# Performance work log

Measured on AMD Instinct MI355X. Metric: run time of the kernel, lower is better.

Reference implementation:

```python
import jax, jax.numpy as jnp
import numpy as np

L = 43          # number of classes
C = L + 3       # <eps>, 'O', 'I-', + L class symbols
B = 128
T = 4096
NEG = jnp.float32(-1e30)


def setup_inputs() -> dict:
    key = jax.random.key(0)
    k1, k2, k3, k4 = jax.random.split(key, 4)
    logits = jax.random.normal(k1, (B, T, C), dtype=jnp.float32)
    log_probs = jax.nn.log_softmax(logits, axis=-1)
    input_lens = jax.random.randint(k2, (B,), T // 2, T + 1).astype(jnp.int32)
    labels = jax.random.randint(k3, (B, T), 1, C).astype(jnp.int32)  # valid (non-eps) symbols
    # den_scores parameter: one raw score per denominator arc (2L+4 arcs).
    # Layout: [0]=0->0 'O', [1:L+1]=0->0 labels, [L+1]=0->1 'I-', [L+2]=0->final,
    #         [L+3]=1->1 'I-', [L+4:2L+4]=1->0 labels.
    den_params = 0.01 * jax.random.normal(k4, (2 * L + 4,), dtype=jnp.float32)
    return {"log_probs": log_probs, "den_params": den_params,
            "input_lens": input_lens, "labels": labels}


def reference(log_probs, den_params, input_lens, labels):
    Bb, Tt, Cc = log_probs.shape
    Ll = Cc - 3
    # set_scores_stochastic_: per-source-state log-softmax of arc scores
    g0 = jax.nn.log_softmax(den_params[: Ll + 3])   # state-0 outgoing arcs
    g1 = jax.nn.log_softmax(den_params[Ll + 3:])    # state-1 outgoing arcs
    s_O, s0_lab, s_0I, s_fin = g0[0], g0[1:Ll + 1], g0[Ll + 1], g0[Ll + 2]
    s_1I, s1_lab = g1[0], g1[1:]

    mask = jnp.arange(Tt)[None, :] < input_lens[:, None]          # [B,T]

    # ---- numerator: linear FSA intersected with emissions = path score ----
    tok_lp = jnp.take_along_axis(log_probs, labels[..., None], axis=-1)[..., 0]
    num = jnp.sum(jnp.where(mask, tok_lp, 0.0), axis=1)           # [B]

    # ---- denominator: log-semiring forward DP over the 2-state topology ----
    lp_t = jnp.moveaxis(log_probs, 1, 0)    # [T,B,C]
    mask_t = jnp.moveaxis(mask, 1, 0)       # [T,B]

    def step(alpha, inputs):
        lp, m = inputs                       # lp [B,C], m [B]
        a0, a1 = alpha[:, 0], alpha[:, 1]
        lp_lab = lp[:, 3:]                   # emissions for class symbols, [B,L]
        # into state 0: 0->0 on 'O', 0->0 on each label, 1->0 on each label
        terms0 = jnp.concatenate([
            (a0 + s_O + lp[:, 1])[:, None],
            a0[:, None] + s0_lab[None, :] + lp_lab,
            a1[:, None] + s1_lab[None, :] + lp_lab,
        ], axis=1)
        n0 = jax.scipy.special.logsumexp(terms0, axis=1)
        # into state 1: 0->1 and 1->1, both on 'I-'
        terms1 = jnp.stack([a0 + s_0I + lp[:, 2], a1 + s_1I + lp[:, 2]], axis=1)
        n1 = jax.scipy.special.logsumexp(terms1, axis=1)
        new = jnp.stack([n0, n1], axis=1)
        new = jnp.where(m[:, None], new, alpha)  # frozen past each seq's length
        return new, None

    alpha0 = jnp.concatenate(
        [jnp.zeros((Bb, 1), log_probs.dtype), jnp.full((Bb, 1), NEG, log_probs.dtype)], axis=1)
    alpha, _ = jax.lax.scan(step, alpha0, (lp_t, mask_t))
    den = alpha[:, 0] + s_fin                                    # final arc 0->2 on -1

    return jnp.sum(num - den)
```

## Files before the change

### kernel.cpp

```cpp
#include <hip/hip_runtime.h>

#define BB 128
#define TT 4096
#define LL 43
#define CC 46
#define CHUNK 64
#define NC (TT / CHUNK)
#define NEGF (-1e30f)
#define L2E 1.44269504088896340736f
#define LN2 0.69314718055994530942f

__device__ __forceinline__ float fexp2(float x) { return __builtin_amdgcn_exp2f(x); }
__device__ __forceinline__ float flog2(float x) { return __builtin_amdgcn_logf(x); }
__device__ __forceinline__ float frcp(float x)  { return __builtin_amdgcn_rcpf(x); }

__global__ __launch_bounds__(64) void crf_chunk(
    const float* __restrict__ lp, const float* __restrict__ dp,
    const int* __restrict__ lens, const int* __restrict__ labels,
    float* __restrict__ res, float* __restrict__ out) {
    __shared__ float tile[CHUNK * CC];
    __shared__ float2 pp[LL + 1];
    __shared__ float sc[4];

    int b = blockIdx.y, c = blockIdx.x;
    int t0 = c * CHUNK;
    int len = lens[b];
    int lane = threadIdx.x;

    if (b == 0 && c == 0 && lane == 0) out[0] = 0.f;

    if (t0 >= len) return;

    {
        const float* gsrc = lp + (size_t)(b * TT + t0) * CC;
        #pragma unroll
        for (int s = 0; s < 11; ++s) {
            const float* g = gsrc + s * 256 + lane * 4;
            float* l = tile + s * 256;
            __builtin_amdgcn_global_load_lds(
                (const __attribute__((address_space(1))) void*)g,
                (__attribute__((address_space(3))) void*)l, 16, 0, 0);
        }
        if (lane < 32) {
            const float* g = gsrc + 11 * 256 + lane * 4;
            float* l = tile + 11 * 256;
            __builtin_amdgcn_global_load_lds(
                (const __attribute__((address_space(1))) void*)g,
                (__attribute__((address_space(3))) void*)l, 16, 0, 0);
        }
    }

    {
        float x0 = (lane < CC) ? dp[lane] : NEGF;
        float x1 = (lane < LL + 1) ? dp[CC + lane] : NEGF;
        float e0 = fexp2(L2E * x0);
        float e1 = fexp2(L2E * x1);
        float s0 = e0, s1 = e1;
        #pragma unroll
        for (int m = 1; m < 64; m <<= 1) {
            s0 += __shfl_xor(s0, m);
            s1 += __shfl_xor(s1, m);
        }
        float r0 = frcp(s0), r1 = frcp(s1);
        float g0 = L2E * x0 - flog2(s0);
        float g1 = L2E * x1 - flog2(s1);
        if (lane >= 1 && lane <= LL) { pp[lane - 1].x = e0 * r0; pp[lane - 1].y = e1 * r1; }
        if (lane == 0) { sc[0] = e0 * r0; sc[2] = g1; }
        if (lane == LL + 1) sc[1] = g0;
    }

    int t = t0 + lane;
    int lab = labels[b * TT + t];
    __syncthreads();

    const float* vr = tile + lane * CC;
    float m00, m01, m10, m11, tok;
    {
        const float2* vr2 = (const float2*)vr;
        float2 c01 = vr2[0];
        float2 c23 = vr2[1];
        tok = vr[lab];
        float w1 = fexp2(L2E * c01.y);
        float v2s = L2E * c23.x;
        float dot0 = sc[0] * w1;
        float dot1 = 0.f;
        {
            float w = fexp2(L2E * c23.y);
            float2 p = pp[0];
            dot0 = fmaf(p.x, w, dot0);
            dot1 = fmaf(p.y, w, dot1);
        }
        #pragma unroll
        for (int k = 2; k <= 22; ++k) {
            float2 v = vr2[k];
            float wa = fexp2(L2E * v.x), wb = fexp2(L2E * v.y);
            float2 pa = pp[2 * k - 3], pb = pp[2 * k - 2];
            dot0 = fmaf(pa.x, wa, dot0); dot1 = fmaf(pa.y, wa, dot1);
            dot0 = fmaf(pb.x, wb, dot0); dot1 = fmaf(pb.y, wb, dot1);
        }
        m00 = dot0;
        m01 = dot1;
        m10 = fexp2(sc[1] + v2s);
        m11 = fexp2(sc[2] + v2s);
    }
    int ie = 0;
    if (t >= len) { m00 = 1.f; m01 = 0.f; m10 = 0.f; m11 = 1.f; tok = 0.f; }

    #pragma unroll
    for (int lev = 0; lev < 6; ++lev) {
        int m = 1 << lev;
        float p00 = __shfl_xor(m00, m), p01 = __shfl_xor(m01, m);
        float p10 = __shfl_xor(m10, m), p11 = __shfl_xor(m11, m);
        int   pe  = __shfl_xor(ie, m);
        float ptk = __shfl_xor(tok, m);
        bool up = (lane & m) != 0;
        float a00 = up ? m00 : p00, a01 = up ? m01 : p01;
        float a10 = up ? m10 : p10, a11 = up ? m11 : p11;
        float b00 = up ? p00 : m00, b01 = up ? p01 : m01;
        float b10 = up ? p10 : m10, b11 = up ? p11 : m11;
        float n00 = fmaf(a01, b10, a00 * b00);
        float n01 = fmaf(a01, b11, a00 * b01);
        float n10 = fmaf(a11, b10, a10 * b00);
        float n11 = fmaf(a11, b11, a10 * b01);
        ie += pe;
        tok += ptk;
        if (lev & 1) {
            float mx = fmaxf(fmaxf(n00, n01), fmaxf(n10, n11));
            unsigned bi = __float_as_uint(mx) >> 23;
            float scl = __uint_as_float((254u - bi) << 23);
            n00 *= scl; n01 *= scl; n10 *= scl; n11 *= scl;
            ie += (int)bi - 127;
        }
        m00 = n00; m01 = n01; m10 = n10; m11 = n11;
    }
    if (lane == 0) {
        float* r = res + (b * NC + c) * 8;
        float fe = (float)ie;
        float4 v = make_float4(flog2(m00) + fe, flog2(m01) + fe,
                               flog2(m10) + fe, flog2(m11) + fe);
        *(float4*)r = v;
        r[4] = tok;
    }
}

__global__ __launch_bounds__(256) void crf_final(
    const float* __restrict__ dp, const int* __restrict__ lens,
    const float* __restrict__ res, float* __restrict__ out) {
    int wv = threadIdx.x >> 6, lane = threadIdx.x & 63;
    int b = blockIdx.x * 4 + wv;
    int len = lens[b];

    float sfin2;
    {
        float x0 = (lane < CC) ? dp[lane] : NEGF;
        float e0 = fexp2(L2E * x0);
        float s0 = e0;
        #pragma unroll
        for (int m = 1; m < 64; m <<= 1) s0 += __shfl_xor(s0, m);
        float g0 = L2E * x0 - flog2(s0);
        sfin2 = __shfl(g0, LL + 2);
    }

    float m00, m01, m10, m11, tok;
    int ie;
    if (lane * CHUNK < len) {
        const float* r = res + (b * NC + lane) * 8;
        float4 rv = *(const float4*)r;
        tok = r[4];
        float rm = fmaxf(fmaxf(rv.x, rv.y), fmaxf(rv.z, rv.w));
        ie = (int)__builtin_floorf(rm);
        float fe = (float)ie;
        m00 = fexp2(rv.x - fe); m01 = fexp2(rv.y - fe);
        m10 = fexp2(rv.z - fe); m11 = fexp2(rv.w - fe);
    } else {
        m00 = 1.f; m01 = 0.f; m10 = 0.f; m11 = 1.f; tok = 0.f; ie = 0;
    }

    #pragma unroll
    for (int m = 1; m < 64; m <<= 1) {
        float p00 = __shfl_xor(m00, m), p01 = __shfl_xor(m01, m);
        float p10 = __shfl_xor(m10, m), p11 = __shfl_xor(m11, m);
        int   pe  = __shfl_xor(ie, m);
        float ptk = __shfl_xor(tok, m);
        bool up = (lane & m) != 0;
        float a00 = up ? m00 : p00, a01 = up ? m01 : p01;
        float a10 = up ? m10 : p10, a11 = up ? m11 : p11;
        float b00 = up ? p00 : m00, b01 = up ? p01 : m01;
        float b10 = up ? p10 : m10, b11 = up ? p11 : m11;
        float n00 = fmaf(a01, b10, a00 * b00);
        float n01 = fmaf(a01, b11, a00 * b01);
        float n10 = fmaf(a11, b10, a10 * b00);
        float n11 = fmaf(a11, b11, a10 * b01);
        float mx = fmaxf(fmaxf(n00, n01), fmaxf(n10, n11));
        unsigned bi = __float_as_uint(mx) >> 23;
        float scl = __uint_as_float((254u - bi) << 23);
        m00 = n00 * scl; m01 = n01 * scl;
        m10 = n10 * scl; m11 = n11 * scl;
        ie = ie + pe + (int)bi - 127;
        tok += ptk;
    }
    if (lane == 0) {
        float den2 = flog2(m00) + (float)ie + sfin2;
        float val = tok - den2 * LN2;
        atomicAdd(out, val);
    }
}

extern "C" void kernel_launch(void* const* d_in, const int* in_sizes, int n_in,
                              void* d_out, int out_size, void* d_ws, size_t ws_size,
                              hipStream_t stream) {
    const float* lp = (const float*)d_in[0];
    const float* dp = (const float*)d_in[1];
    const int* lens = (const int*)d_in[2];
    const int* labels = (const int*)d_in[3];
    float* out = (float*)d_out;
    float* res = (float*)d_ws;

    hipLaunchKernelGGL(crf_chunk, dim3(NC, BB), dim3(64), 0, stream,
                       lp, dp, lens, labels, res, out);
    hipLaunchKernelGGL(crf_final, dim3(BB / 4), dim3(256), 0, stream,
                       dp, lens, res, out);
}
```

Before: 148.1 us.

## Double chunk size per block and pass scaled matrices plus exponent to final

Each block now covers 128 timesteps: 64 lanes handle two rows each, and the two wave-level scan results are combined on lane 0. The intermediate result format changes from log-domain values to mantissa-scaled matrices with an integer exponent, which removes the log and exp conversions in both kernels. This halves the number of blocks and chunk results, so the final kernel's 64-lane reduction maps to 32 valid chunks. The trade-off is less parallelism, with 4096 blocks instead of 8192, and more serial work per wave.

Measured after the change: 152.6 us. 1.03x slower.

```diff
diff --git a/kernel.cpp b/kernel.cpp
--- a/kernel.cpp
+++ b/kernel.cpp
@@ -4,7 +4,7 @@
 #define TT 4096
 #define LL 43
 #define CC 46
-#define CHUNK 64
+#define CHUNK 128
 #define NC (TT / CHUNK)
 #define NEGF (-1e30f)
 #define L2E 1.44269504088896340736f
@@ -34,16 +34,9 @@
     {
         const float* gsrc = lp + (size_t)(b * TT + t0) * CC;
         #pragma unroll
-        for (int s = 0; s < 11; ++s) {
+        for (int s = 0; s < 23; ++s) {
             const float* g = gsrc + s * 256 + lane * 4;
             float* l = tile + s * 256;
-            __builtin_amdgcn_global_load_lds(
-                (const __attribute__((address_space(1))) void*)g,
-                (__attribute__((address_space(3))) void*)l, 16, 0, 0);
-        }
-        if (lane < 32) {
-            const float* g = gsrc + 11 * 256 + lane * 4;
-            float* l = tile + 11 * 256;
             __builtin_amdgcn_global_load_lds(
                 (const __attribute__((address_space(1))) void*)g,
                 (__attribute__((address_space(3))) void*)l, 16, 0, 0);
@@ -69,77 +62,94 @@
         if (lane == LL + 1) sc[1] = g0;
     }
 
-    int t = t0 + lane;
-    int lab = labels[b * TT + t];
+    int lab0 = labels[b * TT + t0 + lane];
+    int lab1 = labels[b * TT + t0 + 64 + lane];
     __syncthreads();
 
-    const float* vr = tile + lane * CC;
-    float m00, m01, m10, m11, tok;
-    {
-        const float2* vr2 = (const float2*)vr;
-        float2 c01 = vr2[0];
-        float2 c23 = vr2[1];
-        tok = vr[lab];
-        float w1 = fexp2(L2E * c01.y);
-        float v2s = L2E * c23.x;
-        float dot0 = sc[0] * w1;
-        float dot1 = 0.f;
+    float A00, A01, A10, A11, Atok; int Aie;
+    float B00, B01, B10, B11, Btok; int Bie;
+
+    #pragma unroll
+    for (int ph = 0; ph < 2; ++ph) {
+        int row = ph * 64 + lane;
+        int t = t0 + row;
+        int lab = ph ? lab1 : lab0;
+        const float* vr = tile + row * CC;
+        float m00, m01, m10, m11, tok;
         {
-            float w = fexp2(L2E * c23.y);
-            float2 p = pp[0];
-            dot0 = fmaf(p.x, w, dot0);
-            dot1 = fmaf(p.y, w, dot1);
-        }
-        #pragma unroll
-        for (int k = 2; k <= 22; ++k) {
-            float2 v = vr2[k];
-            float wa = fexp2(L2E * v.x), wb = fexp2(L2E * v.y);
-            float2 pa = pp[2 * k - 3], pb = pp[2 * k - 2];
-            dot0 = fmaf(pa.x, wa, dot0); dot1 = fmaf(pa.y, wa, dot1);
-            dot0 = fmaf(pb.x, wb, dot0); dot1 = fmaf(pb.y, wb, dot1);
-        }
-        m00 = dot0;
-        m01 = dot1;
-        m10 = fexp2(sc[1] + v2s);
-        m11 = fexp2(sc[2] + v2s);
-    }
-    int ie = 0;
-    if (t >= len) { m00 = 1.f; m01 = 0.f; m10 = 0.f; m11 = 1.f; tok = 0.f; }
-
-    #pragma unroll
-    for (int lev = 0; lev < 6; ++lev) {
-        int m = 1 << lev;
-        float p00 = __shfl_xor(m00, m), p01 = __shfl_xor(m01, m);
-        float p10 = __shfl_xor(m10, m), p11 = __shfl_xor(m11, m);
-        int   pe  = __shfl_xor(ie, m);
-        float ptk = __shfl_xor(tok, m);
-        bool up = (lane & m) != 0;
-        float a00 = up ? m00 : p00, a01 = up ? m01 : p01;
-        float a10 = up ? m10 : p10, a11 = up ? m11 : p11;
-        float b00 = up ? p00 : m00, b01 = up ? p01 : m01;
-        float b10 = up ? p10 : m10, b11 = up ? p11 : m11;
-        float n00 = fmaf(a01, b10, a00 * b00);
-        float n01 = fmaf(a01, b11, a00 * b01);
-        float n10 = fmaf(a11, b10, a10 * b00);
-        float n11 = fmaf(a11, b11, a10 * b01);
-        ie += pe;
-        tok += ptk;
-        if (lev & 1) {
-            float mx = fmaxf(fmaxf(n00, n01), fmaxf(n10, n11));
-            unsigned bi = __float_as_uint(mx) >> 23;
-            float scl = __uint_as_float((254u - bi) << 23);
-            n00 *= scl; n01 *= scl; n10 *= scl; n11 *= scl;
-            ie += (int)bi - 127;
-        }
-        m00 = n00; m01 = n01; m10 = n10; m11 = n11;
-    }
+            const float2* vr2 = (const float2*)vr;
+            float2 c01 = vr2[0];
+            float2 c23 = vr2[1];
+            tok = vr[lab];
+            float w1 = fexp2(L2E * c01.y);
+            float v2s = L2E * c23.x;
+            float dot0 = sc[0] * w1;
+            float dot1 = 0.f;
+            {
+                float w = fexp2(L2E * c23.y);
+                float2 p = pp[0];
+                dot0 = fmaf(p.x, w, dot0);
+                dot1 = fmaf(p.y, w, dot1);
+            }
+            #pragma unroll
+            for (int k = 2; k <= 22; ++k) {
+                float2 v = vr2[k];
+                float wa = fexp2(L2E * v.x), wb = fexp2(L2E * v.y);
+                float2 pa = pp[2 * k - 3], pb = pp[2 * k - 2];
+                dot0 = fmaf(pa.x, wa, dot0); dot1 = fmaf(pa.y, wa, dot1);
+                dot0 = fmaf(pb.x, wb, dot0); dot1 = fmaf(pb.y, wb, dot1);
+            }
+            m00 = dot0;
+            m01 = dot1;
+            m10 = fexp2(sc[1] + v2s);
+            m11 = fexp2(sc[2] + v2s);
+        }
+        int ie = 0;
+        if (t >= len) { m00 = 1.f; m01 = 0.f; m10 = 0.f; m11 = 1.f; tok = 0.f; }
+
+        #pragma unroll
+        for (int lev = 0; lev < 6; ++lev) {
+            int m = 1 << lev;
+            float p00 = __shfl_xor(m00, m), p01 = __shfl_xor(m01, m);
+            float p10 = __shfl_xor(m10, m), p11 = __shfl_xor(m11, m);
+            int   pe  = __shfl_xor(ie, m);
+            float ptk = __shfl_xor(tok, m);
+            bool up = (lane & m) != 0;
+            float a00 = up ? m00 : p00, a01 = up ? m01 : p01;
+            float a10 = up ? m10 : p10, a11 = up ? m11 : p11;
+            float b00 = up ? p00 : m00, b01 = up ? p01 : m01;
+            float b10 = up ? p10 : m10, b11 = up ? p11 : m11;
+            float n00 = fmaf(a01, b10, a00 * b00);
+            float n01 = fmaf(a01, b11, a00 * b01);
+            float n10 = fmaf(a11, b10, a10 * b00);
+            float n11 = fmaf(a11, b11, a10 * b01);
+            ie += pe;
+            tok += ptk;
+            if (lev & 1) {
+                float mx = fmaxf(fmaxf(n00, n01), fmaxf(n10, n11));
+                unsigned bi = __float_as_uint(mx) >> 23;
+                float scl = __uint_as_float((254u - bi) << 23);
+                n00 *= scl; n01 *= scl; n10 *= scl; n11 *= scl;
+                ie += (int)bi - 127;
+            }
+            m00 = n00; m01 = n01; m10 = n10; m11 = n11;
+        }
+        if (ph == 0) { A00 = m00; A01 = m01; A10 = m10; A11 = m11; Atok = tok; Aie = ie; }
+        else         { B00 = m00; B01 = m01; B10 = m10; B11 = m11; Btok = tok; Bie = ie; }
+    }
+
     if (lane == 0) {
+        float n00 = fmaf(B01, A10, B00 * A00);
+        float n01 = fmaf(B01, A11, B00 * A01);
+        float n10 = fmaf(B11, A10, B10 * A00);
+        float n11 = fmaf(B11, A11, B10 * A01);
+        float mx = fmaxf(fmaxf(n00, n01), fmaxf(n10, n11));
+        unsigned bi = __float_as_uint(mx) >> 23;
+        float scl = __uint_as_float((254u - bi) << 23);
+        int ie = Aie + Bie + (int)bi - 127;
         float* r = res + (b * NC + c) * 8;
-        float fe = (float)ie;
-        float4 v = make_float4(flog2(m00) + fe, flog2(m01) + fe,
-                               flog2(m10) + fe, flog2(m11) + fe);
-        *(float4*)r = v;
-        r[4] = tok;
+        *(float4*)r = make_float4(n00 * scl, n01 * scl, n10 * scl, n11 * scl);
+        *(float2*)(r + 4) = make_float2(Atok + Btok, __int_as_float(ie));
     }
 }
 
@@ -166,12 +176,9 @@
     if (lane * CHUNK < len) {
         const float* r = res + (b * NC + lane) * 8;
         float4 rv = *(const float4*)r;
-        tok = r[4];
-        float rm = fmaxf(fmaxf(rv.x, rv.y), fmaxf(rv.z, rv.w));
-        ie = (int)__builtin_floorf(rm);
-        float fe = (float)ie;
-        m00 = fexp2(rv.x - fe); m01 = fexp2(rv.y - fe);
-        m10 = fexp2(rv.z - fe); m11 = fexp2(rv.w - fe);
+        float2 te = *(const float2*)(r + 4);
+        m00 = rv.x; m01 = rv.y; m10 = rv.z; m11 = rv.w;
+        tok = te.x; ie = __float_as_int(te.y);
     } else {
         m00 = 1.f; m01 = 0.f; m10 = 0.f; m11 = 1.f; tok = 0.f; ie = 0;
     }
```
